# Kernel optimization log

Hardware: AMD Instinct MI355X
Metric: run time of the kernel (lower is better)

Reference implementation:

```python
import jax, jax.numpy as jnp
import numpy as np
from jax import lax

D, R, C = 4, 6, 32
P = 2 * R + 1
N = P * P
MR = 12
MP = 2 * MR + 1
MN = MP * MP


def corr_sampler(f_t, f_r, r, dilate):
    # SpatialCorrelationSampler(kernel_size=1, patch_size=2r+1, dilation_patch=dilate)
    # out[b,py,px,y,x] = sum_c f_t[b,c,y,x] * f_r[b,c, y+(py-r)*dilate, x+(px-r)*dilate] (zero pad)
    b, c, h, w = f_t.shape
    p = 2 * r + 1
    pad = r * dilate
    f_r_p = jnp.pad(f_r, ((0, 0), (0, 0), (pad, pad), (pad, pad)))
    offs = jnp.arange(p, dtype=jnp.int32) * dilate
    ii, jj = jnp.meshgrid(offs, offs, indexing='ij')
    shifts = jnp.stack([ii.ravel(), jj.ravel()], 1)  # (p*p, 2)

    def step(_, ij):
        win = lax.dynamic_slice(f_r_p, (0, 0, ij[0], ij[1]), (b, c, h, w))
        return None, jnp.sum(f_t * win, axis=1)  # (b,h,w)

    _, out = lax.scan(step, None, shifts)  # (p*p, b, h, w)
    return out.transpose(1, 0, 2, 3).reshape(b, p, p, h, w)


def bilinear_sample(im, xs, ys):
    # im: (b,c,H,W); xs, ys: (b,h,w) pixel coords; zero padding outside (grid_sample semantics)
    b, c, H, W = im.shape
    x0 = jnp.floor(xs)
    y0 = jnp.floor(ys)
    out = jnp.zeros((b, c) + xs.shape[1:], im.dtype)
    for dy in (0.0, 1.0):
        for dx in (0.0, 1.0):
            xi = x0 + dx
            yi = y0 + dy
            wgt = (1.0 - jnp.abs(xs - xi)) * (1.0 - jnp.abs(ys - yi))
            valid = (xi >= 0) & (xi <= W - 1) & (yi >= 0) & (yi <= H - 1)
            xc = jnp.clip(xi, 0, W - 1).astype(jnp.int32)
            yc = jnp.clip(yi, 0, H - 1).astype(jnp.int32)
            v = jax.vmap(lambda imb, yb, xb: imb[:, yb, xb])(im, yc, xc)  # (b,c,h,w)
            out = out + v * (wgt * valid.astype(im.dtype))[:, None]
    return out


def deform_im2col(im, offset, r):
    # im: (b,c,h,w); offset: (b,h,w,2) with channels (x, y)
    # returns (b, c, (2r+1)^2, h, w), kernel positions row-major over (ky, kx)
    b, c, H, W = im.shape
    h, w = offset.shape[1], offset.shape[2]
    bx = jnp.arange(W, dtype=im.dtype)[None, None, :] + offset[..., 0]  # (b,h,w)
    by = jnp.arange(H, dtype=im.dtype)[None, :, None] + offset[..., 1]
    ks = jnp.arange(-r, r + 1, dtype=im.dtype)
    ky, kx = jnp.meshgrid(ks, ks, indexing='ij')
    koff = jnp.stack([ky.ravel(), kx.ravel()], 1)  # (N, 2) as (ky, kx)

    def step(_, k):
        return None, bilinear_sample(im, bx + k[1], by + k[0])  # (b,c,h,w)

    _, cols = lax.scan(step, None, koff)  # (N,b,c,h,w)
    return cols.transpose(1, 2, 0, 3, 4)


def unfold(x, r):
    # F.unfold(x, kernel_size=2r+1, padding=r) reshaped to (b,c,N,h,w)
    b, c, h, w = x.shape
    p = 2 * r + 1
    xp = jnp.pad(x, ((0, 0), (0, 0), (r, r), (r, r)))
    iy = jnp.arange(p)[:, None] + jnp.arange(h)[None, :]  # (p,h)
    ix = jnp.arange(p)[:, None] + jnp.arange(w)[None, :]  # (p,w)
    win = xp[:, :, iy[:, None, :, None], ix[None, :, None, :]]  # (b,c,p,p,h,w)
    return win.reshape(b, c, p * p, h, w)


def colorizer_forward(feats_r, feats_t, quantized_r, ref_index, current_ind, dil_int):
    ref_list = [int(v) for v in np.asarray(ref_index)]
    nref = feats_r.shape[0]
    gaps = [int(current_ind) - x for x in ref_list]
    nsearch = len([g for g in gaps if g > int(dil_int)])
    dirates = [min(4, g // int(dil_int) + 1) for g in gaps if g > int(dil_int)]
    b, c, h, w = feats_t.shape

    gy, gx = jnp.meshgrid(jnp.arange(-MR, MR + 1, dtype=feats_t.dtype),
                          jnp.arange(-MR, MR + 1, dtype=feats_t.dtype), indexing='ij')
    grid = jnp.stack([gx, gy], -1).reshape(1, MP, MP, 1, 1, 2)

    corrs = []
    offset0 = None
    for i in range(nsearch):
        cc = corr_sampler(feats_t, feats_r[i], MR, dirates[i])  # (b,MP,MP,h,w)
        cc = jax.nn.softmax(cc.reshape(b, MN, h * w), axis=1)
        cc = cc.reshape(b, MP, MP, h, w, 1)
        # expected displacement (x, y); NOTE: original code keeps only the LAST offset0
        offset0 = (cc * grid).sum(axis=(1, 2)) * dirates[i]  # (b,h,w,2)
        col0 = deform_im2col(feats_r[i], offset0, R)  # (b,c,N,h,w)
        corr = (feats_t[:, :, None] * col0).sum(axis=1).reshape(b, N, h * w)
        corrs.append(corr)
    for i in range(nsearch, nref):
        cr = corr_sampler(feats_t, feats_r[i], R, 1).reshape(b, N, h * w)
        corrs.append(cr)

    corr = jax.nn.softmax(jnp.concatenate(corrs, 1), axis=1)[:, None]  # (b,1,nref*N,hw)

    qr = [quantized_r[i][:, :, ::D, ::D] for i in range(nref)]  # prep: stride D (C!=1)
    cols = [deform_im2col(qr[i], offset0, R).reshape(b, C, N, h * w) for i in range(nsearch)]
    cols += [unfold(qr[i], R).reshape(b, C, N, h * w) for i in range(nsearch, nref)]
    image_uf = jnp.concatenate(cols, 2)  # (b,C,nref*N,hw)

    out = (corr * image_uf).sum(axis=2).reshape(b, C, h, w)
    return out


def setup_inputs() -> dict:
    key = jax.random.key(0)
    k1, k2, k3 = jax.random.split(key, 3)
    feats_r = jax.random.normal(k1, (3, 2, 64, 48, 48), jnp.float32) * 0.1
    feats_t = jax.random.normal(k2, (2, 64, 48, 48), jnp.float32) * 0.1
    quantized_r = jax.random.normal(k3, (3, 2, 32, 192, 192), jnp.float32)
    ref_index = np.array([0, 20, 35], dtype=np.int64)
    return {"feats_r": feats_r, "feats_t": feats_t, "quantized_r": quantized_r,
            "ref_index": ref_index, "current_ind": 40, "dil_int": 15}


def reference(feats_r, feats_t, quantized_r, ref_index, current_ind, dil_int):
    return colorizer_forward(feats_r, feats_t, quantized_r, ref_index, current_ind, dil_int)
```

## Files before the change

### kernel.cpp

```cpp
#include <hip/hip_runtime.h>


typedef unsigned short ushort_t;
typedef unsigned int uint_t;
typedef __attribute__((ext_vector_type(8))) short short8;
typedef __attribute__((ext_vector_type(4))) float f32x4;

namespace {
constexpr int NPIX = 2304;
constexpr int FC   = 64;
constexpr int QC   = 32;

constexpr size_t OFS_FTB  = 0;
constexpr size_t OFS_FRB  = OFS_FTB + (size_t)2*NPIX*FC*2;
constexpr size_t OFS_QRCL = OFS_FRB + (size_t)6*NPIX*FC*2;
constexpr size_t OFS_ACC  = OFS_QRCL + (size_t)6*NPIX*QC*4;
constexpr size_t OFS_CORB = OFS_ACC + (size_t)4*NPIX*16*4;
}

__device__ __forceinline__ ushort_t f2b(float f) {
  uint_t u = __float_as_uint(f);
  return (ushort_t)((u + 0x7fffu + ((u >> 16) & 1u)) >> 16);
}

__global__ __launch_bounds__(256) void pack_all(const float* __restrict__ ft,
                                                const float* __restrict__ fr,
                                                const float* __restrict__ q,
                                                ushort_t* __restrict__ ftb,
                                                ushort_t* __restrict__ frb,
                                                float* __restrict__ qrcl) {
  const int bid = blockIdx.x;
  const int tid = threadIdx.x;
  if (bid < 288) {
    __shared__ float lds[64][65];
    const int mat = bid / 36;
    const int p0  = (bid % 36) * 64;
    const float* src = (mat < 2) ? (ft + (size_t)mat * FC * NPIX)
                                 : (fr + (size_t)(mat - 2) * FC * NPIX);
    ushort_t* dst = (mat < 2) ? (ftb + (size_t)mat * NPIX * FC)
                              : (frb + (size_t)(mat - 2) * NPIX * FC);
    const int lane = tid & 63, row = tid >> 6;
    #pragma unroll
    for (int ch = row; ch < 64; ch += 4)
      lds[ch][lane] = src[(size_t)ch * NPIX + p0 + lane];
    __syncthreads();
    #pragma unroll
    for (int p = row; p < 64; p += 4)
      dst[(size_t)(p0 + p) * FC + lane] = f2b(lds[lane][p]);
  } else {
    __shared__ float lq[32][49];
    const int zz = bid - 288;
    const int ib = zz / 48, yy = zz % 48;
    const float* src = q + (size_t)ib * 32 * 36864 + (size_t)(4 * yy) * 192;
    #pragma unroll
    for (int k = 0; k < 6; ++k) {
      const int l = tid + k * 256;
      const int ch = l / 48, xx = l % 48;
      lq[ch][xx] = src[(size_t)ch * 36864 + 4 * xx];
    }
    __syncthreads();
    float* dst = qrcl + ((size_t)ib * NPIX + yy * 48) * QC;
    #pragma unroll
    for (int k = 0; k < 6; ++k) {
      const int o = tid + k * 256;
      dst[o] = lq[o & 31][o >> 5];
    }
  }
}

template<int MODE>
__device__ __forceinline__ void gram_body(const ushort_t* __restrict__ ftb,
                                          const ushort_t* __restrict__ frb,
                                          float* __restrict__ accb,
                                          float* __restrict__ corb,
                                          int y, int m0, int b, int chunk,
                                          int c0, int c1) {
  constexpr int D_  = (MODE == 0) ? 3 : (MODE == 1) ? 2 : 1;
  constexpr int RAD = (MODE == 2) ? 6 : 12;

  const int lane = threadIdx.x;
  const int col  = lane & 15;
  const int kg   = lane >> 4;

  const short8* ftv = (const short8*)(ftb + ((size_t)b * NPIX + y * 48 + m0 + col) * FC);
  short8 aF0 = ftv[kg];
  short8 aF1 = ftv[4 + kg];

  float wm[3][4], dxv[3][4];
  int sbase[3][4];
  #pragma unroll
  for (int nt = 0; nt < 3; ++nt) {
    #pragma unroll
    for (int r = 0; r < 4; ++r) {
      const int xr   = m0 + kg * 4 + r;
      const int diff = nt * 16 + col - xr;
      const int qd   = diff / D_;
      const bool v   = (diff % D_ == 0) && (qd >= -RAD) && (qd <= RAD);
      wm[nt][r]  = v ? 1.f : 0.f;
      dxv[nt][r] = (float)qd;
      if (MODE == 2) sbase[nt][r] = ((int)b * NPIX + y * 48 + xr) * 169 + (qd + 6);
    }
  }

  const ushort_t* frmat = frb + (size_t)(MODE * 2 + b) * NPIX * FC;
  float se[4] = {0,0,0,0}, sx[4] = {0,0,0,0}, sy[4] = {0,0,0,0};

  for (int dy = c0; dy < c1; ++dy) {
    const int yyr = y + (dy - RAD) * D_;
    if (yyr < 0 || yyr >= 48) continue;
    const float dyv = (float)(dy - RAD);
    const short8* frow = (const short8*)(frmat + (size_t)yyr * 48 * FC);
    #pragma unroll
    for (int nt = 0; nt < 3; ++nt) {
      const short8* bp = frow + (size_t)(nt * 16 + col) * 8;
      short8 b0 = bp[kg], b1 = bp[4 + kg];
      f32x4 c = {0.f, 0.f, 0.f, 0.f};
      c = __builtin_amdgcn_mfma_f32_16x16x32_bf16(aF0, b0, c, 0, 0, 0);
      c = __builtin_amdgcn_mfma_f32_16x16x32_bf16(aF1, b1, c, 0, 0, 0);
      if (MODE < 2) {
        #pragma unroll
        for (int r = 0; r < 4; ++r) {
          const float e = __expf(c[r]) * wm[nt][r];
          se[r] += e;
          sx[r] = fmaf(e, dxv[nt][r], sx[r]);
          sy[r] = fmaf(e, dyv, sy[r]);
        }
      } else {
        #pragma unroll
        for (int r = 0; r < 4; ++r)
          if (wm[nt][r] != 0.f) corb[sbase[nt][r] + dy * 13] = c[r];
      }
    }
  }

  if (MODE < 2) {
    #pragma unroll
    for (int r = 0; r < 4; ++r) {
      #pragma unroll
      for (int m = 1; m <= 8; m <<= 1) {
        se[r] += __shfl_xor(se[r], m);
        sx[r] += __shfl_xor(sx[r], m);
        sy[r] += __shfl_xor(sy[r], m);
      }
    }
    if (col == 0) {
      #pragma unroll
      for (int r = 0; r < 4; ++r) {
        const int p = y * 48 + m0 + kg * 4 + r;
        float* a = accb + ((size_t)(MODE * 2 + b) * NPIX + p) * 16 + chunk * 3;
        a[0] = se[r]; a[1] = sx[r]; a[2] = sy[r];
      }
    }
  }
}

__global__ __launch_bounds__(64) void gram_kernel(const ushort_t* __restrict__ ftb,
                                                  const ushort_t* __restrict__ frb,
                                                  float* __restrict__ accb,
                                                  float* __restrict__ corb) {
  const int y  = blockIdx.x;
  const int m0 = blockIdx.y * 16;
  const int z  = blockIdx.z;
  if (z < 10) {
    const int b = z / 5, chunk = z % 5;
    gram_body<0>(ftb, frb, accb, corb, y, m0, b, chunk, chunk * 5, chunk * 5 + 5);
  } else if (z < 20) {
    const int zz = z - 10;
    const int b = zz / 5, chunk = zz % 5;
    gram_body<1>(ftb, frb, accb, corb, y, m0, b, chunk, chunk * 5, chunk * 5 + 5);
  } else {
    const int zz = z - 20;
    const int b = zz / 3, chunk = zz % 3;
    const int c0 = (chunk == 0) ? 0 : (chunk == 1) ? 5 : 9;
    const int c1 = (chunk == 0) ? 5 : (chunk == 1) ? 9 : 13;
    gram_body<2>(ftb, frb, accb, corb, y, m0, b, chunk, c0, c1);
  }
}

__global__ __launch_bounds__(128, 6) void fuse_kernel(const ushort_t* __restrict__ ftb,
                                                      const ushort_t* __restrict__ frb,
                                                      const float* __restrict__ accb,
                                                      const float* __restrict__ corb,
                                                      const float* __restrict__ qrcl,
                                                      float* __restrict__ out) {
  const int tid = threadIdx.x;
  const int wv = tid >> 6, lane = tid & 63;
  const int b = blockIdx.y;
  const int pix = blockIdx.x * 2 + wv;
  const int x = pix % 48, y = pix / 48;

  __shared__ __align__(16) float sDu[2][416];
  __shared__ float sp[2][512];
  __shared__ int   gaddr[2][224];
  __shared__ float gw0[2][224], gw1[2][224];

  const int kgB = lane >> 4;
  const short8* ftv = (const short8*)(ftb + ((size_t)b * NPIX + pix) * FC);
  const short8 bF0 = ftv[kgB], bF1 = ftv[4 + kgB];

  float cv5 = 0.f, cv6 = 0.f, cv7 = 0.f;
  {
    const float* cb = corb + ((size_t)b * NPIX + pix) * 169;
    int n = lane - 18;
    if (n >= 0) {
      const int yy = y + n / 13 - 6, xx = x + n % 13 - 6;
      if (yy >= 0 && yy < 48 && xx >= 0 && xx < 48) cv5 = cb[n];
    }
    n = lane + 46;
    {
      const int yy = y + n / 13 - 6, xx = x + n % 13 - 6;
      if (yy >= 0 && yy < 48 && xx >= 0 && xx < 48) cv6 = cb[n];
    }
    n = lane + 110;
    if (n < 169) {
      const int yy = y + n / 13 - 6, xx = x + n % 13 - 6;
      if (yy >= 0 && yy < 48 && xx >= 0 && xx < 48) cv7 = cb[n];
    }
  }

  float vox = 0.f, voy = 0.f;
  if (lane < 2) {
    const int d = (lane == 0) ? 3 : 2;
    const float4* a4 = (const float4*)(accb + ((size_t)(lane * 2 + b) * NPIX + pix) * 16);
    float t[16];
    *(float4*)&t[0]  = a4[0]; *(float4*)&t[4]  = a4[1];
    *(float4*)&t[8]  = a4[2]; *(float4*)&t[12] = a4[3];
    float se = t[0] + t[3] + t[6] + t[9] + t[12];
    float sx = t[1] + t[4] + t[7] + t[10] + t[13];
    float sy = t[2] + t[5] + t[8] + t[11] + t[14];
    const int klox = max(-12, -(x / d)), khix = min(12, (47 - x) / d);
    const int kloy = max(-12, -(y / d)), khiy = min(12, (47 - y) / d);
    const int nvx = khix - klox + 1, nvy = khiy - kloy + 1;
    const int svx = (klox + khix) * nvx / 2, svy = (kloy + khiy) * nvy / 2;
    se += (float)(625 - nvx * nvy);
    sx -= (float)(nvy * svx);
    sy -= (float)(nvx * svy);
    vox = (float)d * sx / se;
    voy = (float)d * sy / se;
  }
  const float ox0 = __shfl(vox, 0), oy0 = __shfl(voy, 0);
  const float ox1 = __shfl(vox, 1), oy1 = __shfl(voy, 1);

  const float bxf0 = floorf((float)x + ox0), byf0 = floorf((float)y + oy0);
  const float bxf1 = floorf((float)x + ox1), byf1 = floorf((float)y + oy1);
  const float fx0 = (float)x + ox0 - bxf0, fy0 = (float)y + oy0 - byf0;
  const float fx1 = (float)x + ox1 - bxf1, fy1 = (float)y + oy1 - byf1;
  const int bx00 = (int)bxf0 - 6, by00 = (int)byf0 - 6;
  const int bx01 = (int)bxf1 - 6, by01 = (int)byf1 - 6;

  {
    const int arow = lane & 15, kg = lane >> 4;
    const short8 z8 = {0,0,0,0,0,0,0,0};
    float* sDw = sDu[wv];
    #pragma unroll 2
    for (int gi = 0; gi < 26; ++gi) {
      const bool r1 = gi >= 13;
      const int grp = r1 ? gi - 13 : gi;
      const int g = grp * 16 + arow;
      short8 a0 = z8, a1 = z8;
      if (g < 196) {
        const int gy = (r1 ? by01 : by00) + g / 14;
        const int gx = (r1 ? bx01 : bx00) + g % 14;
        if (gy >= 0 && gy < 48 && gx >= 0 && gx < 48) {
          const short8* fp = (const short8*)(frb + ((size_t)((r1 ? 2 : 0) + b) * NPIX + gy * 48 + gx) * FC);
          a0 = fp[kg]; a1 = fp[4 + kg];
        }
      }
      f32x4 c = {0.f, 0.f, 0.f, 0.f};
      c = __builtin_amdgcn_mfma_f32_16x16x32_bf16(a0, bF0, c, 0, 0, 0);
      c = __builtin_amdgcn_mfma_f32_16x16x32_bf16(a1, bF1, c, 0, 0, 0);
      if (arow == 0)
        *(f32x4*)&sDw[(r1 ? 208 : 0) + grp * 16 + kg * 4] = c;
    }
  }
  __syncthreads();

  float ls = 0.f;
  {
    float* spw = sp[wv];
    const float* sD0 = sDu[wv];
    const float* sD1 = sDu[wv] + 208;
    #pragma unroll
    for (int k = 0; k < 8; ++k) {
      const int s = lane + 64 * k;
      if (s < 507) {
        float v;
        if (s < 338) {
          const bool r1 = (s >= 169);
          const unsigned n = r1 ? s - 169 : s;
          const float fx = r1 ? fx1 : fx0, fy = r1 ? fy1 : fy0;
          const float w00 = (1.f - fy) * (1.f - fx), w01 = (1.f - fy) * fx;
          const float w10 = fy * (1.f - fx),        w11 = fy * fx;
          const unsigned a_ = n / 13u, c2 = n % 13u;
          const float* Dp = r1 ? sD1 : sD0;
          v = w00 * Dp[a_ * 14 + c2]       + w01 * Dp[a_ * 14 + c2 + 1]
            + w10 * Dp[(a_ + 1) * 14 + c2] + w11 * Dp[(a_ + 1) * 14 + c2 + 1];
        } else {
          v = (k == 5) ? cv5 : (k == 6) ? cv6 : cv7;
        }
        const float e = __expf(v);
        spw[s] = e; ls += e;
      }
    }
  }
  #pragma unroll
  for (int o = 1; o <= 32; o <<= 1) ls += __shfl_xor(ls, o);
  const float inv = 1.f / ls;
  __syncthreads();

  int*   gaddr2 = (int*)sDu[wv];
  float* gwq2   = sDu[wv] + 208;
  {
    const float* spw = sp[wv];
    const float w00 = (1.f - fy1) * (1.f - fx1), w01 = (1.f - fy1) * fx1;
    const float w10 = fy1 * (1.f - fx1),        w11 = fy1 * fx1;
    #pragma unroll
    for (int j = 0; j < 4; ++j) {
      const int t = lane + 64 * j;
      if (t < 224) {
        if (t < 196) {
          const int ty = t / 14, tx = t % 14;
          auto P = [&](const float* base, int a, int c2) -> float {
            return (a >= 0 && a < 13 && c2 >= 0 && c2 < 13) ? base[a * 13 + c2] : 0.f;
          };
          const float s0 = w00 * P(spw, ty, tx)     + w01 * P(spw, ty, tx - 1)
                         + w10 * P(spw, ty - 1, tx) + w11 * P(spw, ty - 1, tx - 1);
          const float s1 = w00 * P(spw + 169, ty, tx)     + w01 * P(spw + 169, ty, tx - 1)
                         + w10 * P(spw + 169, ty - 1, tx) + w11 * P(spw + 169, ty - 1, tx - 1);
          const int gy = by01 + ty, gx = bx01 + tx;
          const bool v = (gy >= 0 && gy < 48 && gx >= 0 && gx < 48);
          gaddr[wv][t] = v ? (gy * 48 + gx) * QC : 0;
          gw0[wv][t] = v ? s0 : 0.f;
          gw1[wv][t] = v ? s1 : 0.f;
        } else {
          gaddr[wv][t] = 0; gw0[wv][t] = 0.f; gw1[wv][t] = 0.f;
        }
      }
    }
    #pragma unroll
    for (int j = 0; j < 3; ++j) {
      const int t = lane + 64 * j;
      if (t < 169) {
        const int yy = y + t / 13 - 6, xx = x + t % 13 - 6;
        const bool v = (yy >= 0 && yy < 48 && xx >= 0 && xx < 48);
        gaddr2[t] = v ? (yy * 48 + xx) * QC : 0;
        gwq2[t] = v ? spw[338 + t] : 0.f;
      } else {
        gaddr2[t] = 0; gwq2[t] = 0.f;
      }
    }
  }
  __syncthreads();

  const int chgrp = lane & 7, ssub = lane >> 3;
  const float* q0 = qrcl + (size_t)(0 + b) * NPIX * QC + chgrp * 4;
  const float* q1 = qrcl + (size_t)(2 + b) * NPIX * QC + chgrp * 4;
  const float* q2 = qrcl + (size_t)(4 + b) * NPIX * QC + chgrp * 4;
  float4 acc = {0.f, 0.f, 0.f, 0.f};
  const int* ga = gaddr[wv];
  const float* w0p = gw0[wv];
  const float* w1p = gw1[wv];
  #pragma unroll 4
  for (int it = 0; it < 28; ++it) {
    const int s = it * 8 + ssub;
    const int a = ga[s];
    const float w0 = w0p[s], w1 = w1p[s];
    const float4 v0 = *(const float4*)(q0 + a);
    const float4 v1 = *(const float4*)(q1 + a);
    acc.x = fmaf(w0, v0.x, acc.x); acc.y = fmaf(w0, v0.y, acc.y);
    acc.z = fmaf(w0, v0.z, acc.z); acc.w = fmaf(w0, v0.w, acc.w);
    acc.x = fmaf(w1, v1.x, acc.x); acc.y = fmaf(w1, v1.y, acc.y);
    acc.z = fmaf(w1, v1.z, acc.z); acc.w = fmaf(w1, v1.w, acc.w);
  }
  #pragma unroll 4
  for (int it = 0; it < 24; ++it) {
    const int s = it * 8 + ssub;
    const int a = gaddr2[s];
    const float w = gwq2[s];
    const float4 v2 = *(const float4*)(q2 + a);
    acc.x = fmaf(w, v2.x, acc.x); acc.y = fmaf(w, v2.y, acc.y);
    acc.z = fmaf(w, v2.z, acc.z); acc.w = fmaf(w, v2.w, acc.w);
  }
  #pragma unroll
  for (int off = 8; off <= 32; off <<= 1) {
    acc.x += __shfl_xor(acc.x, off);
    acc.y += __shfl_xor(acc.y, off);
    acc.z += __shfl_xor(acc.z, off);
    acc.w += __shfl_xor(acc.w, off);
  }
  if (ssub == 0) {
    float* op = out + ((size_t)(b * 32 + chgrp * 4) * 48 + y) * 48 + x;
    op[0]        = acc.x * inv;
    op[NPIX]     = acc.y * inv;
    op[2 * NPIX] = acc.z * inv;
    op[3 * NPIX] = acc.w * inv;
  }
}

extern "C" void kernel_launch(void* const* d_in, const int* in_sizes, int n_in,
                              void* d_out, int out_size, void* d_ws, size_t ws_size,
                              hipStream_t stream) {
  (void)in_sizes; (void)n_in; (void)out_size; (void)ws_size;
  const float* feats_r     = (const float*)d_in[0];
  const float* feats_t     = (const float*)d_in[1];
  const float* quantized_r = (const float*)d_in[2];
  char* ws = (char*)d_ws;
  ushort_t* ftb  = (ushort_t*)(ws + OFS_FTB);
  ushort_t* frb  = (ushort_t*)(ws + OFS_FRB);
  float*    qrcl = (float*)(ws + OFS_QRCL);
  float*    accb = (float*)(ws + OFS_ACC);
  float*    corb = (float*)(ws + OFS_CORB);

  pack_all<<<576, 256, 0, stream>>>(feats_t, feats_r, quantized_r, ftb, frb, qrcl);
  gram_kernel<<<dim3(48, 3, 26), 64, 0, stream>>>(ftb, frb, accb, corb);
  fuse_kernel<<<dim3(NPIX / 2, 2), 128, 0, stream>>>(ftb, frb, accb, corb, qrcl, (float*)d_out);
}
```

Before: 140.7 us.

## Compute third-reference local correlation inside fuse kernel instead of gram kernel

The 13x13 local correlation for the third reference was computed in the gram kernel and stored to a global scratch buffer, then reloaded by the fuse kernel. Now the fuse kernel computes it directly with extra MFMA groups (11 more tiles) into enlarged shared memory, removing the scratch buffer write/read and 6 z-slices of the gram launch. The trade-off is more per-pixel MFMA work and gathers in the fuse kernel, plus more shared memory, which may lower occupancy.

```diff
diff --git a/kernel.cpp b/kernel.cpp
--- a/kernel.cpp
+++ b/kernel.cpp
@@ -15,7 +15,6 @@
 constexpr size_t OFS_FRB  = OFS_FTB + (size_t)2*NPIX*FC*2;
 constexpr size_t OFS_QRCL = OFS_FRB + (size_t)6*NPIX*FC*2;
 constexpr size_t OFS_ACC  = OFS_QRCL + (size_t)6*NPIX*QC*4;
-constexpr size_t OFS_CORB = OFS_ACC + (size_t)4*NPIX*16*4;
 }
 
 __device__ __forceinline__ ushort_t f2b(float f) {
@@ -72,11 +71,10 @@
 __device__ __forceinline__ void gram_body(const ushort_t* __restrict__ ftb,
                                           const ushort_t* __restrict__ frb,
                                           float* __restrict__ accb,
-                                          float* __restrict__ corb,
                                           int y, int m0, int b, int chunk,
                                           int c0, int c1) {
-  constexpr int D_  = (MODE == 0) ? 3 : (MODE == 1) ? 2 : 1;
-  constexpr int RAD = (MODE == 2) ? 6 : 12;
+  constexpr int D_  = (MODE == 0) ? 3 : 2;
+  constexpr int RAD = 12;
 
   const int lane = threadIdx.x;
   const int col  = lane & 15;
@@ -87,7 +85,6 @@
   short8 aF1 = ftv[4 + kg];
 
   float wm[3][4], dxv[3][4];
-  int sbase[3][4];
   #pragma unroll
   for (int nt = 0; nt < 3; ++nt) {
     #pragma unroll
@@ -98,7 +95,6 @@
       const bool v   = (diff % D_ == 0) && (qd >= -RAD) && (qd <= RAD);
       wm[nt][r]  = v ? 1.f : 0.f;
       dxv[nt][r] = (float)qd;
-      if (MODE == 2) sbase[nt][r] = ((int)b * NPIX + y * 48 + xr) * 169 + (qd + 6);
     }
   }
 
@@ -117,70 +113,54 @@
       f32x4 c = {0.f, 0.f, 0.f, 0.f};
       c = __builtin_amdgcn_mfma_f32_16x16x32_bf16(aF0, b0, c, 0, 0, 0);
       c = __builtin_amdgcn_mfma_f32_16x16x32_bf16(aF1, b1, c, 0, 0, 0);
-      if (MODE < 2) {
-        #pragma unroll
-        for (int r = 0; r < 4; ++r) {
-          const float e = __expf(c[r]) * wm[nt][r];
-          se[r] += e;
-          sx[r] = fmaf(e, dxv[nt][r], sx[r]);
-          sy[r] = fmaf(e, dyv, sy[r]);
-        }
-      } else {
-        #pragma unroll
-        for (int r = 0; r < 4; ++r)
-          if (wm[nt][r] != 0.f) corb[sbase[nt][r] + dy * 13] = c[r];
-      }
-    }
-  }
-
-  if (MODE < 2) {
-    #pragma unroll
-    for (int r = 0; r < 4; ++r) {
-      #pragma unroll
-      for (int m = 1; m <= 8; m <<= 1) {
-        se[r] += __shfl_xor(se[r], m);
-        sx[r] += __shfl_xor(sx[r], m);
-        sy[r] += __shfl_xor(sy[r], m);
-      }
-    }
-    if (col == 0) {
       #pragma unroll
       for (int r = 0; r < 4; ++r) {
-        const int p = y * 48 + m0 + kg * 4 + r;
-        float* a = accb + ((size_t)(MODE * 2 + b) * NPIX + p) * 16 + chunk * 3;
-        a[0] = se[r]; a[1] = sx[r]; a[2] = sy[r];
-      }
+        const float e = __expf(c[r]) * wm[nt][r];
+        se[r] += e;
+        sx[r] = fmaf(e, dxv[nt][r], sx[r]);
+        sy[r] = fmaf(e, dyv, sy[r]);
+      }
+    }
+  }
+
+  #pragma unroll
+  for (int r = 0; r < 4; ++r) {
+    #pragma unroll
+    for (int m = 1; m <= 8; m <<= 1) {
+      se[r] += __shfl_xor(se[r], m);
+      sx[r] += __shfl_xor(sx[r], m);
+      sy[r] += __shfl_xor(sy[r], m);
+    }
+  }
+  if (col == 0) {
+    #pragma unroll
+    for (int r = 0; r < 4; ++r) {
+      const int p = y * 48 + m0 + kg * 4 + r;
+      float* a = accb + ((size_t)(MODE * 2 + b) * NPIX + p) * 16 + chunk * 3;
+      a[0] = se[r]; a[1] = sx[r]; a[2] = sy[r];
     }
   }
 }
 
 __global__ __launch_bounds__(64) void gram_kernel(const ushort_t* __restrict__ ftb,
                                                   const ushort_t* __restrict__ frb,
-                                                  float* __restrict__ accb,
-                                                  float* __restrict__ corb) {
+                                                  float* __restrict__ accb) {
   const int y  = blockIdx.x;
   const int m0 = blockIdx.y * 16;
   const int z  = blockIdx.z;
   if (z < 10) {
     const int b = z / 5, chunk = z % 5;
-    gram_body<0>(ftb, frb, accb, corb, y, m0, b, chunk, chunk * 5, chunk * 5 + 5);
-  } else if (z < 20) {
+    gram_body<0>(ftb, frb, accb, y, m0, b, chunk, chunk * 5, chunk * 5 + 5);
+  } else {
     const int zz = z - 10;
     const int b = zz / 5, chunk = zz % 5;
-    gram_body<1>(ftb, frb, accb, corb, y, m0, b, chunk, chunk * 5, chunk * 5 + 5);
-  } else {
-    const int zz = z - 20;
-    const int b = zz / 3, chunk = zz % 3;
-    const int c0 = (chunk == 0) ? 0 : (chunk == 1) ? 5 : 9;
-    const int c1 = (chunk == 0) ? 5 : (chunk == 1) ? 9 : 13;
-    gram_body<2>(ftb, frb, accb, corb, y, m0, b, chunk, c0, c1);
+    gram_body<1>(ftb, frb, accb, y, m0, b, chunk, chunk * 5, chunk * 5 + 5);
   }
 }
 
 __global__ __launch_bounds__(128, 6) void fuse_kernel(const ushort_t* __restrict__ ftb,
                                                       const ushort_t* __restrict__ frb,
                                                       const float* __restrict__ accb,
-                                                      const float* __restrict__ corb,
                                                       const float* __restrict__ qrcl,
                                                       float* __restrict__ out) {
   const int tid = threadIdx.x;
@@ -189,7 +169,7 @@
   const int pix = blockIdx.x * 2 + wv;
   const int x = pix % 48, y = pix / 48;
 
-  __shared__ __align__(16) float sDu[2][416];
+  __shared__ __align__(16) float sDu[2][592];
   __shared__ float sp[2][512];
   __shared__ int   gaddr[2][224];
   __shared__ float gw0[2][224], gw1[2][224];
@@ -197,26 +177,6 @@
   const int kgB = lane >> 4;
   const short8* ftv = (const short8*)(ftb + ((size_t)b * NPIX + pix) * FC);
   const short8 bF0 = ftv[kgB], bF1 = ftv[4 + kgB];
-
-  float cv5 = 0.f, cv6 = 0.f, cv7 = 0.f;
-  {
-    const float* cb = corb + ((size_t)b * NPIX + pix) * 169;
-    int n = lane - 18;
-    if (n >= 0) {
-      const int yy = y + n / 13 - 6, xx = x + n % 13 - 6;
-      if (yy >= 0 && yy < 48 && xx >= 0 && xx < 48) cv5 = cb[n];
-    }
-    n = lane + 46;
-    {
-      const int yy = y + n / 13 - 6, xx = x + n % 13 - 6;
-      if (yy >= 0 && yy < 48 && xx >= 0 && xx < 48) cv6 = cb[n];
-    }
-    n = lane + 110;
-    if (n < 169) {
-      const int yy = y + n / 13 - 6, xx = x + n % 13 - 6;
-      if (yy >= 0 && yy < 48 && xx >= 0 && xx < 48) cv7 = cb[n];
-    }
-  }
 
   float vox = 0.f, voy = 0.f;
   if (lane < 2) {
@@ -253,24 +213,37 @@
     const short8 z8 = {0,0,0,0,0,0,0,0};
     float* sDw = sDu[wv];
     #pragma unroll 2
-    for (int gi = 0; gi < 26; ++gi) {
-      const bool r1 = gi >= 13;
-      const int grp = r1 ? gi - 13 : gi;
-      const int g = grp * 16 + arow;
+    for (int gi = 0; gi < 37; ++gi) {
+      int refb, base, gy, gx, maxg, g;
+      if (gi < 26) {
+        const bool r1 = gi >= 13;
+        const int grp = r1 ? gi - 13 : gi;
+        g = grp * 16 + arow;
+        refb = r1 ? 2 : 0;
+        base = r1 ? 208 : 0;
+        gy = (r1 ? by01 : by00) + (int)((unsigned)g / 14u);
+        gx = (r1 ? bx01 : bx00) + (int)((unsigned)g % 14u);
+        maxg = 196;
+        base += grp * 16;
+      } else {
+        const int grp = gi - 26;
+        g = grp * 16 + arow;
+        refb = 4;
+        base = 416 + grp * 16;
+        gy = y + (int)((unsigned)g / 13u) - 6;
+        gx = x + (int)((unsigned)g % 13u) - 6;
+        maxg = 169;
+      }
       short8 a0 = z8, a1 = z8;
-      if (g < 196) {
-        const int gy = (r1 ? by01 : by00) + g / 14;
-        const int gx = (r1 ? bx01 : bx00) + g % 14;
-        if (gy >= 0 && gy < 48 && gx >= 0 && gx < 48) {
-          const short8* fp = (const short8*)(frb + ((size_t)((r1 ? 2 : 0) + b) * NPIX + gy * 48 + gx) * FC);
-          a0 = fp[kg]; a1 = fp[4 + kg];
-        }
+      if (g < maxg && gy >= 0 && gy < 48 && gx >= 0 && gx < 48) {
+        const short8* fp = (const short8*)(frb + ((size_t)(refb + b) * NPIX + gy * 48 + gx) * FC);
+        a0 = fp[kg]; a1 = fp[4 + kg];
       }
       f32x4 c = {0.f, 0.f, 0.f, 0.f};
       c = __builtin_amdgcn_mfma_f32_16x16x32_bf16(a0, bF0, c, 0, 0, 0);
       c = __builtin_amdgcn_mfma_f32_16x16x32_bf16(a1, bF1, c, 0, 0, 0);
       if (arow == 0)
-        *(f32x4*)&sDw[(r1 ? 208 : 0) + grp * 16 + kg * 4] = c;
+        *(f32x4*)&sDw[base + kg * 4] = c;
     }
   }
   __syncthreads();
@@ -280,6 +253,7 @@
     float* spw = sp[wv];
     const float* sD0 = sDu[wv];
     const float* sD1 = sDu[wv] + 208;
+    const float* sD2 = sDu[wv] + 416;
     #pragma unroll
     for (int k = 0; k < 8; ++k) {
       const int s = lane + 64 * k;
@@ -296,7 +270,7 @@
           v = w00 * Dp[a_ * 14 + c2]       + w01 * Dp[a_ * 14 + c2 + 1]
             + w10 * Dp[(a_ + 1) * 14 + c2] + w11 * Dp[(a_ + 1) * 14 + c2 + 1];
         } else {
-          v = (k == 5) ? cv5 : (k == 6) ? cv6 : cv7;
+          v = sD2[s - 338];
         }
         const float e = __expf(v);
         spw[s] = e; ls += e;
@@ -409,9 +383,8 @@
   ushort_t* frb  = (ushort_t*)(ws + OFS_FRB);
   float*    qrcl = (float*)(ws + OFS_QRCL);
   float*    accb = (float*)(ws + OFS_ACC);
-  float*    corb = (float*)(ws + OFS_CORB);
 
   pack_all<<<576, 256, 0, stream>>>(feats_t, feats_r, quantized_r, ftb, frb, qrcl);
-  gram_kernel<<<dim3(48, 3, 26), 64, 0, stream>>>(ftb, frb, accb, corb);
-  fuse_kernel<<<dim3(NPIX / 2, 2), 128, 0, stream>>>(ftb, frb, accb, corb, qrcl, (float*)d_out);
-}
+  gram_kernel<<<dim3(48, 3, 20), 64, 0, stream>>>(ftb, frb, accb);
+  fuse_kernel<<<dim3(NPIX / 2, 2), 128, 0, stream>>>(ftb, frb, accb, qrcl, (float*)d_out);
+}
```

After: 145.5 us. +3.4%, slower.
